# Performance work log

Hardware: AMD Instinct MI355X
Metric: run time of the kernel (lower is better)

## Reference

```python
import jax, jax.numpy as jnp
import numpy as np
from jax.ops import segment_sum, segment_max

N_NODES = 50000
N_GRAPHS = 64
EPS = 1e-16


def gat_layer(x, src, dst, W, a_src, a_dst, b, n_nodes):
    # PyG GATConv, heads=1: shared linear, additive attention, per-dst softmax
    h = x @ W                                  # [N, H]
    al_s = h @ a_src                           # [N]
    al_d = h @ a_dst                           # [N]
    e = jax.nn.leaky_relu(al_s[src] + al_d[dst], 0.2)   # [E]
    # numerically stable segment softmax over edges grouped by dst
    m = segment_max(e, dst, num_segments=n_nodes)
    m = jnp.where(jnp.isfinite(m), m, 0.0)
    ex = jnp.exp(e - m[dst])
    denom = segment_sum(ex, dst, num_segments=n_nodes)
    alpha = ex / (denom[dst] + EPS)            # [E]
    out = segment_sum(alpha[:, None] * h[src], dst, num_segments=n_nodes)
    return out + b


def setup_inputs() -> dict:
    key = jax.random.key(0)
    ks = jax.random.split(key, 16)
    H = 128
    x = jax.random.normal(ks[0], (N_NODES, 4), dtype=jnp.float32)
    edge_index = jax.random.randint(ks[1], (2, 800000), 0, N_NODES, dtype=jnp.int64)
    batch = jnp.sort(jax.random.randint(ks[2], (N_NODES,), 0, N_GRAPHS, dtype=jnp.int64))

    def glorot(k, shape):
        lim = np.sqrt(6.0 / (shape[0] + shape[-1]))
        return jax.random.uniform(k, shape, jnp.float32, -lim, lim)

    params = {
        'W1': glorot(ks[3], (4, H)), 'as1': glorot(ks[4], (H,)), 'ad1': glorot(ks[5], (H,)), 'b1': jnp.zeros((H,), jnp.float32),
        'W2': glorot(ks[6], (H, H)), 'as2': glorot(ks[7], (H,)), 'ad2': glorot(ks[8], (H,)), 'b2': jnp.zeros((H,), jnp.float32),
        'W3': glorot(ks[9], (H, H)), 'as3': glorot(ks[10], (H,)), 'ad3': glorot(ks[11], (H,)), 'b3': jnp.zeros((H,), jnp.float32),
        'Wlin': glorot(ks[12], (H, 2)), 'blin': jnp.zeros((2,), jnp.float32),
    }
    return {'x': x, 'edge_index': edge_index, 'batch': batch, **params}


def reference(x, edge_index, batch, W1, as1, ad1, b1, W2, as2, ad2, b2, W3, as3, ad3, b3, Wlin, blin):
    n = x.shape[0]
    # GATConv default add_self_loops=True
    loop = jnp.arange(n, dtype=edge_index.dtype)
    src = jnp.concatenate([edge_index[0], loop])
    dst = jnp.concatenate([edge_index[1], loop])

    h = jax.nn.relu(gat_layer(x, src, dst, W1, as1, ad1, b1, n))
    h = jax.nn.relu(gat_layer(h, src, dst, W2, as2, ad2, b2, n))
    h = gat_layer(h, src, dst, W3, as3, ad3, b3, n)

    # global_mean_pool
    sums = segment_sum(h, batch, num_segments=N_GRAPHS)          # [G, H]
    cnt = segment_sum(jnp.ones((n,), h.dtype), batch, num_segments=N_GRAPHS)
    pooled = sums / jnp.maximum(cnt, 1.0)[:, None]
    # dropout p=0.5 is identity in eval mode
    return pooled @ Wlin + blin                                   # [G, 2]
```

## Files before the change

### kernel.cpp

```cpp
#include <hip/hip_runtime.h>
#include <math.h>


#define BW 512
#define PART_CHUNK 4096

typedef __attribute__((ext_vector_type(8))) short short8v;
typedef __attribute__((ext_vector_type(4))) float f32x4;

__device__ __forceinline__ float bflo(unsigned u) { return __uint_as_float(u << 16); }
__device__ __forceinline__ float bfhi(unsigned u) { return __uint_as_float(u & 0xffff0000u); }
__device__ __forceinline__ unsigned pk2bf(float a, float b) {
  unsigned ua = __float_as_uint(a); ua += 0x7fffu + ((ua >> 16) & 1u);
  unsigned ub = __float_as_uint(b); ub += 0x7fffu + ((ub >> 16) & 1u);
  return (ua >> 16) | (ub & 0xffff0000u);
}

__global__ __launch_bounds__(256) void kb_hist(const int* __restrict__ ei,
                                               int* __restrict__ bcnt,
                                               int E, int ET, int NB) {
  __shared__ int h[128];
  int tid = threadIdx.x;
  if (tid < 128) h[tid] = 0;
  __syncthreads();
  int stride = gridDim.x * 256;
  for (int i = blockIdx.x * 256 + tid; i < ET; i += stride) {
    int dst = (i < E) ? ei[E + i] : (i - E);
    atomicAdd(&h[dst >> 9], 1);
  }
  __syncthreads();
  if (tid < NB && h[tid] > 0) atomicAdd(&bcnt[tid], h[tid]);
}

__global__ __launch_bounds__(128) void kb_scan(const int* __restrict__ bcnt,
                                               int* __restrict__ bbase,
                                               int* __restrict__ bcur,
                                               int* __restrict__ rowp,
                                               int N, int ET, int NB) {
  __shared__ int sm[128];
  int t = threadIdx.x;
  int v = (t < NB) ? bcnt[t] : 0;
  sm[t] = v;
  __syncthreads();
  for (int off = 1; off < 128; off <<= 1) {
    int u = (t >= off) ? sm[t - off] : 0;
    __syncthreads();
    sm[t] += u;
    __syncthreads();
  }
  int pre = sm[t] - v;
  if (t <= NB) bbase[t] = pre;
  if (t < NB) bcur[t] = pre;
  if (t == 0) rowp[N] = ET;
}

__global__ __launch_bounds__(256) void kb_part(const int* __restrict__ ei,
                                               int* __restrict__ bcur,
                                               int* __restrict__ bucketed,
                                               int E, int ET, int NB) {
  __shared__ int hist[128];
  __shared__ int runb[128];
  int tid = threadIdx.x;
  int base = blockIdx.x * PART_CHUNK;
  if (tid < 128) hist[tid] = 0;

  int sv[16], dv[16];
#pragma unroll
  for (int k = 0; k < 16; ++k) {
    int j = base + k * 256 + tid;
    int s = -1, d = 0;
    if (j < ET) {
      if (j < E) { s = ei[j]; d = ei[E + j]; }
      else       { s = j - E; d = j - E; }
    }
    sv[k] = s; dv[k] = d;
  }
  __syncthreads();
#pragma unroll
  for (int k = 0; k < 16; ++k)
    if (sv[k] >= 0) atomicAdd(&hist[dv[k] >> 9], 1);
  __syncthreads();
  if (tid < NB && hist[tid] > 0) runb[tid] = atomicAdd(&bcur[tid], hist[tid]);
  __syncthreads();
  if (tid < 128) hist[tid] = 0;
  __syncthreads();
#pragma unroll
  for (int k = 0; k < 16; ++k) {
    if (sv[k] >= 0) {
      int b = dv[k] >> 9;
      int off = atomicAdd(&hist[b], 1);
      bucketed[runb[b] + off] = (sv[k] << 9) | (dv[k] & (BW - 1));
    }
  }
}

__global__ __launch_bounds__(256) void kb_csr(const int* __restrict__ bucketed,
                                              const int* __restrict__ bbase,
                                              int* __restrict__ rowp,
                                              int* __restrict__ csr,
                                              int N) {
  __shared__ int h[512];
  __shared__ int sm[256];
  __shared__ int cur[512];
  int tid = threadIdx.x;
  int b = blockIdx.x;
  int cb = bbase[b], ce = bbase[b + 1];

  h[tid] = 0; h[tid + 256] = 0;
  __syncthreads();
  for (int j = cb + tid; j < ce; j += 256)
    atomicAdd(&h[bucketed[j] & (BW - 1)], 1);
  __syncthreads();
  int a0 = h[2 * tid], a1 = h[2 * tid + 1];
  int s = a0 + a1;
  sm[tid] = s;
  __syncthreads();
  for (int off = 1; off < 256; off <<= 1) {
    int u = (tid >= off) ? sm[tid - off] : 0;
    __syncthreads();
    sm[tid] += u;
    __syncthreads();
  }
  int pre = sm[tid] - s;
  cur[2 * tid] = pre;
  cur[2 * tid + 1] = pre + a0;
  __syncthreads();
  int node0 = b * BW;
  for (int local = tid; local < BW; local += 256) {
    int node = node0 + local;
    if (node < N) rowp[node] = cb + cur[local];
  }
  __syncthreads();
  for (int j = cb + tid; j < ce; j += 256) {
    int p = bucketed[j];
    int loc = p & (BW - 1);
    int pos = cb + atomicAdd(&cur[loc], 1);
    csr[pos] = (unsigned)p >> 9;
  }
}

__global__ __launch_bounds__(256) void k_prep(const float* __restrict__ W2,
                                              const float* __restrict__ W3,
                                              unsigned short* __restrict__ Wcm2,
                                              unsigned short* __restrict__ Wcm3) {
  int i = blockIdx.x * 256 + threadIdx.x;
  if (i < 16384) {
    int k = i >> 7, n = i & 127;
    unsigned u = __float_as_uint(W2[i]); u += 0x7fffu + ((u >> 16) & 1u);
    Wcm2[n * 128 + k] = (unsigned short)(u >> 16);
    unsigned v = __float_as_uint(W3[i]); v += 0x7fffu + ((v >> 16) & 1u);
    Wcm3[n * 128 + k] = (unsigned short)(v >> 16);
  }
}

__global__ __launch_bounds__(64) void k_al1(const float* __restrict__ W1,
                                            const float* __restrict__ as1,
                                            const float* __restrict__ ad1,
                                            float* __restrict__ wv) {
  int lane = threadIdx.x;
  float2 a = *(const float2*)(as1 + lane * 2);
  float2 d = *(const float2*)(ad1 + lane * 2);
  float ps[4], pd[4];
#pragma unroll
  for (int k = 0; k < 4; ++k) {
    float2 w = *(const float2*)(W1 + k * 128 + lane * 2);
    ps[k] = w.x * a.x + w.y * a.y;
    pd[k] = w.x * d.x + w.y * d.y;
  }
  for (int off = 32; off; off >>= 1) {
#pragma unroll
    for (int k = 0; k < 4; ++k) {
      ps[k] += __shfl_xor(ps[k], off);
      pd[k] += __shfl_xor(pd[k], off);
    }
  }
  if (lane == 0) {
#pragma unroll
    for (int k = 0; k < 4; ++k) { wv[k] = ps[k]; wv[4 + k] = pd[k]; }
  }
}

__global__ __launch_bounds__(256) void k_alnode(const float* __restrict__ X,
                                                const float* __restrict__ wv,
                                                float* __restrict__ al_s,
                                                float* __restrict__ al_d, int N) {
  int i = blockIdx.x * 256 + threadIdx.x;
  if (i >= N) return;
  float4 xv = *(const float4*)(X + i * 4);
  al_s[i] = xv.x * wv[0] + xv.y * wv[1] + xv.z * wv[2] + xv.w * wv[3];
  al_d[i] = xv.x * wv[4] + xv.y * wv[5] + xv.z * wv[6] + xv.w * wv[7];
}

__global__ __launch_bounds__(256) void k_aggx(const int* __restrict__ csr_src,
                                              const int* __restrict__ rowp,
                                              const float* __restrict__ al_s,
                                              const float* __restrict__ al_d,
                                              const float* __restrict__ X,
                                              float* __restrict__ exw,
                                              float* __restrict__ AX, int N) {
  int wid = threadIdx.x >> 6, lane = threadIdx.x & 63;
  int dst = blockIdx.x * 4 + wid;
  if (dst >= N) return;
  int beg = rowp[dst], end = rowp[dst + 1];
  int deg = end - beg;
  float ald = al_d[dst];
  float4 acc = {0.f, 0.f, 0.f, 0.f};

  if (deg <= 64) {
    int srcv = 0;
    float e = -INFINITY;
    if (lane < deg) {
      srcv = csr_src[beg + lane];
      e = al_s[srcv] + ald;
      e = (e > 0.f) ? e : 0.2f * e;
    }
    float m = e;
    for (int off = 32; off; off >>= 1) m = fmaxf(m, __shfl_xor(m, off));
    float av = (lane < deg) ? __expf(e - m) : 0.f;
    float den = av;
    for (int off = 32; off; off >>= 1) den += __shfl_xor(den, off);
    av *= 1.0f / (den + 1e-16f);
    float4 xv = {0.f, 0.f, 0.f, 0.f};
    if (lane < deg) xv = *(const float4*)(X + (size_t)srcv * 4);
    acc.x = av * xv.x; acc.y = av * xv.y; acc.z = av * xv.z; acc.w = av * xv.w;
  } else {
    float m = -INFINITY;
    for (int j = beg + lane; j < end; j += 64) {
      float e = al_s[csr_src[j]] + ald;
      e = (e > 0.f) ? e : 0.2f * e;
      exw[j] = e;
      m = fmaxf(m, e);
    }
    for (int off = 32; off; off >>= 1) m = fmaxf(m, __shfl_xor(m, off));
    float den = 0.f;
    for (int j = beg + lane; j < end; j += 64) {
      float ex = __expf(exw[j] - m);
      exw[j] = ex;
      den += ex;
    }
    for (int off = 32; off; off >>= 1) den += __shfl_xor(den, off);
    float inv = 1.0f / (den + 1e-16f);
    for (int j = beg + lane; j < end; j += 64) {
      int s = csr_src[j];
      float w = exw[j] * inv;
      float4 xv = *(const float4*)(X + (size_t)s * 4);
      acc.x += w * xv.x; acc.y += w * xv.y; acc.z += w * xv.z; acc.w += w * xv.w;
    }
  }
  for (int off = 32; off; off >>= 1) {
    acc.x += __shfl_xor(acc.x, off);
    acc.y += __shfl_xor(acc.y, off);
    acc.z += __shfl_xor(acc.z, off);
    acc.w += __shfl_xor(acc.w, off);
  }
  if (lane == 0) *(float4*)(AX + (size_t)dst * 4) = acc;
}

__global__ __launch_bounds__(256) void k_gemm4b(const float* __restrict__ AX,
                                                const float* __restrict__ W,
                                                const float* __restrict__ bias,
                                                unsigned* __restrict__ Ybf, int N) {
  int wid = threadIdx.x >> 6, lane = threadIdx.x & 63;
  int node = blockIdx.x * 4 + wid;
  if (node >= N) return;
  float4 xv = *(const float4*)(AX + (size_t)node * 4);
  int f = lane * 2;
  float2 w0 = *(const float2*)(W + f);
  float2 w1 = *(const float2*)(W + 128 + f);
  float2 w2 = *(const float2*)(W + 256 + f);
  float2 w3 = *(const float2*)(W + 384 + f);
  float2 bv = *(const float2*)(bias + f);
  float h0 = xv.x * w0.x + xv.y * w1.x + xv.z * w2.x + xv.w * w3.x + bv.x;
  float h1 = xv.x * w0.y + xv.y * w1.y + xv.z * w2.y + xv.w * w3.y + bv.y;
  h0 = fmaxf(h0, 0.f); h1 = fmaxf(h1, 0.f);
  Ybf[(size_t)node * 64 + lane] = pk2bf(h0, h1);
}

__global__ __launch_bounds__(256) void k_gemm128mfma(
    const unsigned short* __restrict__ Xbf,
    const unsigned short* __restrict__ Wcm,
    const float* __restrict__ asv, const float* __restrict__ adv,
    unsigned* __restrict__ Hbf,
    float* __restrict__ al_s, float* __restrict__ al_d, int N) {
  int wid = threadIdx.x >> 6, lane = threadIdx.x & 63;
  int c = lane & 15, g = lane >> 4;
  int row0 = blockIdx.x * 64 + wid * 16;
  int arow = row0 + c;
  int arowc = (arow < N) ? arow : (N - 1);

  short8v a[4];
#pragma unroll
  for (int kt = 0; kt < 4; ++kt)
    a[kt] = *(const short8v*)(Xbf + (size_t)arowc * 128 + kt * 32 + g * 8);

  f32x4 acc[8];
#pragma unroll
  for (int f = 0; f < 8; ++f) acc[f] = (f32x4){0.f, 0.f, 0.f, 0.f};

#pragma unroll
  for (int f = 0; f < 8; ++f) {
    const unsigned short* wb = Wcm + (size_t)(f * 16 + c) * 128 + g * 8;
#pragma unroll
    for (int kt = 0; kt < 4; ++kt) {
      short8v b = *(const short8v*)(wb + kt * 32);
      acc[f] = __builtin_amdgcn_mfma_f32_16x16x32_bf16(a[kt], b, acc[f], 0, 0, 0);
    }
  }

  float ps[4] = {0.f, 0.f, 0.f, 0.f}, pd[4] = {0.f, 0.f, 0.f, 0.f};
#pragma unroll
  for (int f = 0; f < 8; ++f) {
    float as_c = asv[f * 16 + c], ad_c = adv[f * 16 + c];
#pragma unroll
    for (int j = 0; j < 4; ++j) { ps[j] += acc[f][j] * as_c; pd[j] += acc[f][j] * ad_c; }
  }
#pragma unroll
  for (int j = 0; j < 4; ++j) {
    for (int off = 1; off < 16; off <<= 1) {
      ps[j] += __shfl_xor(ps[j], off);
      pd[j] += __shfl_xor(pd[j], off);
    }
  }
  if (c == 0) {
#pragma unroll
    for (int j = 0; j < 4; ++j) {
      int r = row0 + g * 4 + j;
      if (r < N) { al_s[r] = ps[j]; al_d[r] = pd[j]; }
    }
  }

#pragma unroll
  for (int f = 0; f < 8; ++f) {
#pragma unroll
    for (int j = 0; j < 4; ++j) {
      float partner = __shfl_xor(acc[f][j], 1);
      int r = row0 + g * 4 + j;
      if (((lane & 1) == 0) && r < N)
        Hbf[(size_t)r * 64 + f * 8 + (c >> 1)] = pk2bf(acc[f][j], partner);
    }
  }
}

__global__ __launch_bounds__(256) void k_agg(const int* __restrict__ csr_src,
                                             const int* __restrict__ rowp,
                                             const float* __restrict__ al_s,
                                             const float* __restrict__ al_d,
                                             const uint4* __restrict__ Hbf,
                                             const float* __restrict__ bias,
                                             float* __restrict__ exw,
                                             float* __restrict__ Yf32,
                                             uint4* __restrict__ Ybf,
                                             int N, int relu) {
  int wid = threadIdx.x >> 6, lane = threadIdx.x & 63;
  int dst = blockIdx.x * 4 + wid;
  if (dst >= N) return;
  int beg = rowp[dst], end = rowp[dst + 1];
  int deg = end - beg;
  float ald = al_d[dst];

  int q = lane >> 4;
  int l = lane & 15;
  float acc[8];
#pragma unroll
  for (int c = 0; c < 8; ++c) acc[c] = 0.f;

  if (deg <= 64) {
    int srcv = 0;
    float e = -INFINITY;
    if (lane < deg) {
      srcv = csr_src[beg + lane];
      e = al_s[srcv] + ald;
      e = (e > 0.f) ? e : 0.2f * e;
    }
    float m = e;
    for (int off = 32; off; off >>= 1) m = fmaxf(m, __shfl_xor(m, off));
    float av = (lane < deg) ? __expf(e - m) : 0.f;
    float den = av;
    for (int off = 32; off; off >>= 1) den += __shfl_xor(den, off);
    av *= 1.0f / (den + 1e-16f);

    int t = 0;
    for (; t + 16 <= deg; t += 16) {
      int s0 = __shfl(srcv, t + q);
      int s1 = __shfl(srcv, t + 4 + q);
      int s2 = __shfl(srcv, t + 8 + q);
      int s3 = __shfl(srcv, t + 12 + q);
      float w0 = __shfl(av, t + q);
      float w1 = __shfl(av, t + 4 + q);
      float w2 = __shfl(av, t + 8 + q);
      float w3 = __shfl(av, t + 12 + q);
      uint4 v0 = Hbf[(size_t)s0 * 16 + l];
      uint4 v1 = Hbf[(size_t)s1 * 16 + l];
      uint4 v2 = Hbf[(size_t)s2 * 16 + l];
      uint4 v3 = Hbf[(size_t)s3 * 16 + l];
      acc[0] += w0 * bflo(v0.x) + w1 * bflo(v1.x) + w2 * bflo(v2.x) + w3 * bflo(v3.x);
      acc[1] += w0 * bfhi(v0.x) + w1 * bfhi(v1.x) + w2 * bfhi(v2.x) + w3 * bfhi(v3.x);
      acc[2] += w0 * bflo(v0.y) + w1 * bflo(v1.y) + w2 * bflo(v2.y) + w3 * bflo(v3.y);
      acc[3] += w0 * bfhi(v0.y) + w1 * bfhi(v1.y) + w2 * bfhi(v2.y) + w3 * bfhi(v3.y);
      acc[4] += w0 * bflo(v0.z) + w1 * bflo(v1.z) + w2 * bflo(v2.z) + w3 * bflo(v3.z);
      acc[5] += w0 * bfhi(v0.z) + w1 * bfhi(v1.z) + w2 * bfhi(v2.z) + w3 * bfhi(v3.z);
      acc[6] += w0 * bflo(v0.w) + w1 * bflo(v1.w) + w2 * bflo(v2.w) + w3 * bflo(v3.w);
      acc[7] += w0 * bfhi(v0.w) + w1 * bfhi(v1.w) + w2 * bfhi(v2.w) + w3 * bfhi(v3.w);
    }
    if (t + 8 <= deg) {
      int sA = __shfl(srcv, t + q);
      int sB = __shfl(srcv, t + 4 + q);
      float wA = __shfl(av, t + q);
      float wB = __shfl(av, t + 4 + q);
      uint4 va = Hbf[(size_t)sA * 16 + l];
      uint4 vb = Hbf[(size_t)sB * 16 + l];
      acc[0] += wA * bflo(va.x) + wB * bflo(vb.x);
      acc[1] += wA * bfhi(va.x) + wB * bfhi(vb.x);
      acc[2] += wA * bflo(va.y) + wB * bflo(vb.y);
      acc[3] += wA * bfhi(va.y) + wB * bfhi(vb.y);
      acc[4] += wA * bflo(va.z) + wB * bflo(vb.z);
      acc[5] += wA * bfhi(va.z) + wB * bfhi(vb.z);
      acc[6] += wA * bflo(va.w) + wB * bflo(vb.w);
      acc[7] += wA * bfhi(va.w) + wB * bfhi(vb.w);
      t += 8;
    }
    if (t + 4 <= deg) {
      int sA = __shfl(srcv, t + q);
      float wA = __shfl(av, t + q);
      uint4 va = Hbf[(size_t)sA * 16 + l];
      acc[0] += wA * bflo(va.x); acc[1] += wA * bfhi(va.x);
      acc[2] += wA * bflo(va.y); acc[3] += wA * bfhi(va.y);
      acc[4] += wA * bflo(va.z); acc[5] += wA * bfhi(va.z);
      acc[6] += wA * bflo(va.w); acc[7] += wA * bfhi(va.w);
      t += 4;
    }
    {
      int sA = __shfl(srcv, t + q);
      float wA = __shfl(av, t + q);
      if (t + q < deg) {
        uint4 va = Hbf[(size_t)sA * 16 + l];
        acc[0] += wA * bflo(va.x); acc[1] += wA * bfhi(va.x);
        acc[2] += wA * bflo(va.y); acc[3] += wA * bfhi(va.y);
        acc[4] += wA * bflo(va.z); acc[5] += wA * bfhi(va.z);
        acc[6] += wA * bflo(va.w); acc[7] += wA * bfhi(va.w);
      }
    }
  } else {
    float m = -INFINITY;
    for (int j = beg + lane; j < end; j += 64) {
      float e = al_s[csr_src[j]] + ald;
      e = (e > 0.f) ? e : 0.2f * e;
      exw[j] = e;
      m = fmaxf(m, e);
    }
    for (int off = 32; off; off >>= 1) m = fmaxf(m, __shfl_xor(m, off));

    float den = 0.f;
    for (int j = beg + lane; j < end; j += 64) {
      float ex = __expf(exw[j] - m);
      exw[j] = ex;
      den += ex;
    }
    for (int off = 32; off; off >>= 1) den += __shfl_xor(den, off);
    float inv = 1.0f / (den + 1e-16f);

    for (int j = beg + q; j < end; j += 4) {
      int sA = csr_src[j];
      float wA = exw[j] * inv;
      uint4 va = Hbf[(size_t)sA * 16 + l];
      acc[0] += wA * bflo(va.x); acc[1] += wA * bfhi(va.x);
      acc[2] += wA * bflo(va.y); acc[3] += wA * bfhi(va.y);
      acc[4] += wA * bflo(va.z); acc[5] += wA * bfhi(va.z);
      acc[6] += wA * bflo(va.w); acc[7] += wA * bfhi(va.w);
    }
  }

#pragma unroll
  for (int c = 0; c < 8; ++c) {
    acc[c] += __shfl_xor(acc[c], 16);
    acc[c] += __shfl_xor(acc[c], 32);
  }
  if (q == 0) {
    float4 bv0 = *(const float4*)(bias + l * 8);
    float4 bv1 = *(const float4*)(bias + l * 8 + 4);
    float o0 = acc[0] + bv0.x, o1 = acc[1] + bv0.y, o2 = acc[2] + bv0.z, o3 = acc[3] + bv0.w;
    float o4 = acc[4] + bv1.x, o5 = acc[5] + bv1.y, o6 = acc[6] + bv1.z, o7 = acc[7] + bv1.w;
    if (relu) {
      o0 = fmaxf(o0, 0.f); o1 = fmaxf(o1, 0.f); o2 = fmaxf(o2, 0.f); o3 = fmaxf(o3, 0.f);
      o4 = fmaxf(o4, 0.f); o5 = fmaxf(o5, 0.f); o6 = fmaxf(o6, 0.f); o7 = fmaxf(o7, 0.f);
      uint4 pb;
      pb.x = pk2bf(o0, o1); pb.y = pk2bf(o2, o3);
      pb.z = pk2bf(o4, o5); pb.w = pk2bf(o6, o7);
      Ybf[(size_t)dst * 16 + l] = pb;
    } else {
      float4 w0 = make_float4(o0, o1, o2, o3);
      float4 w1 = make_float4(o4, o5, o6, o7);
      *(float4*)(Yf32 + (size_t)dst * 128 + l * 8) = w0;
      *(float4*)(Yf32 + (size_t)dst * 128 + l * 8 + 4) = w1;
    }
  }
}

__global__ __launch_bounds__(256) void k_pool(const float* __restrict__ Hh,
                                              const int* __restrict__ batch,
                                              float* __restrict__ gsum,
                                              float* __restrict__ gcnt,
                                              int N, int nwaves) {
  int gw = (blockIdx.x * 256 + threadIdx.x) >> 6;
  int lane = threadIdx.x & 63;
  int chunk = (N + nwaves - 1) / nwaves;
  int beg = gw * chunk;
  int end = beg + chunk; if (end > N) end = N;
  if (beg >= end) return;

  int curg = batch[beg];
  float2 acc = {0.f, 0.f};
  int cnt = 0;
  for (int n = beg; n < end; ++n) {
    int g = batch[n];
    if (g != curg) {
      atomicAdd(&gsum[curg * 128 + lane * 2], acc.x);
      atomicAdd(&gsum[curg * 128 + lane * 2 + 1], acc.y);
      if (lane == 0) atomicAdd(&gcnt[curg], (float)cnt);
      acc.x = 0.f; acc.y = 0.f; cnt = 0; curg = g;
    }
    float2 h = *(const float2*)(Hh + (size_t)n * 128 + lane * 2);
    acc.x += h.x; acc.y += h.y; ++cnt;
  }
  atomicAdd(&gsum[curg * 128 + lane * 2], acc.x);
  atomicAdd(&gsum[curg * 128 + lane * 2 + 1], acc.y);
  if (lane == 0) atomicAdd(&gcnt[curg], (float)cnt);
}

__global__ __launch_bounds__(128) void k_final(const float* __restrict__ gsum,
                                               const float* __restrict__ gcnt,
                                               const float* __restrict__ Wlin,
                                               const float* __restrict__ blin,
                                               float* __restrict__ out) {
  int t = threadIdx.x;
  int g = t >> 1, c = t & 1;
  float inv = 1.0f / fmaxf(gcnt[g], 1.0f);
  float acc = blin[c];
  for (int k = 0; k < 128; ++k) acc += gsum[g * 128 + k] * inv * Wlin[k * 2 + c];
  out[g * 2 + c] = acc;
}

extern "C" void kernel_launch(void* const* d_in, const int* in_sizes, int n_in,
                              void* d_out, int out_size, void* d_ws, size_t ws_size,
                              hipStream_t stream) {
  const float* x    = (const float*)d_in[0];
  const int*   ei   = (const int*)d_in[1];
  const int*   batch= (const int*)d_in[2];
  const float* W1   = (const float*)d_in[3];
  const float* as1  = (const float*)d_in[4];
  const float* ad1  = (const float*)d_in[5];
  const float* b1   = (const float*)d_in[6];
  const float* W2   = (const float*)d_in[7];
  const float* as2  = (const float*)d_in[8];
  const float* ad2  = (const float*)d_in[9];
  const float* b2   = (const float*)d_in[10];
  const float* W3   = (const float*)d_in[11];
  const float* as3  = (const float*)d_in[12];
  const float* ad3  = (const float*)d_in[13];
  const float* b3   = (const float*)d_in[14];
  const float* Wlin = (const float*)d_in[15];
  const float* blin = (const float*)d_in[16];

  int N = in_sizes[0] / 4;
  int E = in_sizes[1] / 2;
  int ET = E + N;
  int NB = (N + BW - 1) / BW;

  char* ws = (char*)d_ws;
  unsigned* bfA = (unsigned*)ws; ws += (size_t)N * 64 * 4;
  unsigned* bfB = (unsigned*)ws; ws += (size_t)N * 64 * 4;
  float* bufY = (float*)ws; ws += (size_t)N * 128 * 4;
  float* al_s = (float*)ws; ws += (size_t)N * 4;
  float* al_d = (float*)ws; ws += (size_t)N * 4;
  float* AX   = (float*)ws; ws += (size_t)N * 4 * 4;
  float* gsum = (float*)ws; ws += (size_t)64 * 128 * 4;
  float* gcnt = (float*)ws; ws += (size_t)64 * 4;
  float* wv   = (float*)ws; ws += (size_t)64 * 4;
  int* rowp   = (int*)ws;   ws += (size_t)(N + 1) * 4;
  int* csr    = (int*)ws;   ws += (size_t)ET * 4;
  float* exw  = (float*)ws; ws += (size_t)ET * 4;
  int* bucketed = (int*)ws; ws += (size_t)ET * 4;
  int* bcnt   = (int*)ws;   ws += (size_t)128 * 4;
  int* bbase  = (int*)ws;   ws += (size_t)132 * 4;
  int* bcur   = (int*)ws;   ws += (size_t)128 * 4;
  unsigned short* wcm2 = (unsigned short*)ws; ws += (size_t)128 * 128 * 2;
  unsigned short* wcm3 = (unsigned short*)ws; ws += (size_t)128 * 128 * 2;

  hipMemsetAsync(bcnt, 0, (size_t)128 * 4, stream);
  hipMemsetAsync(gsum, 0, (size_t)(64 * 128 + 64) * 4, stream);

  kb_hist<<<256, 256, 0, stream>>>(ei, bcnt, E, ET, NB);
  kb_scan<<<1, 128, 0, stream>>>(bcnt, bbase, bcur, rowp, N, ET, NB);
  kb_part<<<(ET + PART_CHUNK - 1) / PART_CHUNK, 256, 0, stream>>>(ei, bcur, bucketed, E, ET, NB);
  kb_csr <<<NB, 256, 0, stream>>>(bucketed, bbase, rowp, csr, N);
  k_prep <<<64, 256, 0, stream>>>(W2, W3, wcm2, wcm3);
  k_al1  <<<1, 64, 0, stream>>>(W1, as1, ad1, wv);

  int nb4 = (N + 3) / 4;
  int nb64 = (N + 63) / 64;
  k_alnode<<<(N + 255) / 256, 256, 0, stream>>>(x, wv, al_s, al_d, N);
  k_aggx  <<<nb4, 256, 0, stream>>>(csr, rowp, al_s, al_d, x, exw, AX, N);
  k_gemm4b<<<nb4, 256, 0, stream>>>(AX, W1, b1, bfB, N);
  k_gemm128mfma<<<nb64, 256, 0, stream>>>((const unsigned short*)bfB, wcm2, as2, ad2, bfA, al_s, al_d, N);
  k_agg        <<<nb4, 256, 0, stream>>>(csr, rowp, al_s, al_d, (const uint4*)bfA, b2, exw, bufY, (uint4*)bfB, N, 1);
  k_gemm128mfma<<<nb64, 256, 0, stream>>>((const unsigned short*)bfB, wcm3, as3, ad3, bfA, al_s, al_d, N);
  k_agg        <<<nb4, 256, 0, stream>>>(csr, rowp, al_s, al_d, (const uint4*)bfA, b3, exw, bufY, (uint4*)bfB, N, 0);

  k_pool <<<256, 256, 0, stream>>>(bufY, batch, gsum, gcnt, N, 1024);
  k_final<<<1, 128, 0, stream>>>(gsum, gcnt, Wlin, blin, (float*)d_out);
}
```

Before: 330.7 us.

## Fuse layer-1 gather with its linear, merge prep kernels, fuse pool and head

Folds the k_al1 wave into an extra block of k_prep and fuses layer-1 aggregation with the 4-to-128 linear, which removes the AX round trip and two launches. The final layer now writes bf16 instead of fp32, roughly halving that output's traffic. The atomic pool and final head kernels become one per-graph kernel that binary-searches the sorted batch array, so the memset and atomics go away. In exchange, pooling runs on bf16 activations at lower precision, and each graph is summed by a single block of 256 threads, which limits parallelism.

```diff
diff --git a/kernel.cpp b/kernel.cpp
--- a/kernel.cpp
+++ b/kernel.cpp
@@ -141,8 +141,37 @@
 
 __global__ __launch_bounds__(256) void k_prep(const float* __restrict__ W2,
                                               const float* __restrict__ W3,
+                                              const float* __restrict__ W1,
+                                              const float* __restrict__ as1,
+                                              const float* __restrict__ ad1,
                                               unsigned short* __restrict__ Wcm2,
-                                              unsigned short* __restrict__ Wcm3) {
+                                              unsigned short* __restrict__ Wcm3,
+                                              float* __restrict__ wv) {
+  if (blockIdx.x == 64) {
+    int lane = threadIdx.x;
+    if (lane >= 64) return;
+    float2 a = *(const float2*)(as1 + lane * 2);
+    float2 d = *(const float2*)(ad1 + lane * 2);
+    float ps[4], pd[4];
+#pragma unroll
+    for (int k = 0; k < 4; ++k) {
+      float2 w = *(const float2*)(W1 + k * 128 + lane * 2);
+      ps[k] = w.x * a.x + w.y * a.y;
+      pd[k] = w.x * d.x + w.y * d.y;
+    }
+    for (int off = 32; off; off >>= 1) {
+#pragma unroll
+      for (int k = 0; k < 4; ++k) {
+        ps[k] += __shfl_xor(ps[k], off);
+        pd[k] += __shfl_xor(pd[k], off);
+      }
+    }
+    if (lane == 0) {
+#pragma unroll
+      for (int k = 0; k < 4; ++k) { wv[k] = ps[k]; wv[4 + k] = pd[k]; }
+    }
+    return;
+  }
   int i = blockIdx.x * 256 + threadIdx.x;
   if (i < 16384) {
     int k = i >> 7, n = i & 127;
@@ -150,33 +179,6 @@
     Wcm2[n * 128 + k] = (unsigned short)(u >> 16);
     unsigned v = __float_as_uint(W3[i]); v += 0x7fffu + ((v >> 16) & 1u);
     Wcm3[n * 128 + k] = (unsigned short)(v >> 16);
-  }
-}
-
-__global__ __launch_bounds__(64) void k_al1(const float* __restrict__ W1,
-                                            const float* __restrict__ as1,
-                                            const float* __restrict__ ad1,
-                                            float* __restrict__ wv) {
-  int lane = threadIdx.x;
-  float2 a = *(const float2*)(as1 + lane * 2);
-  float2 d = *(const float2*)(ad1 + lane * 2);
-  float ps[4], pd[4];
-#pragma unroll
-  for (int k = 0; k < 4; ++k) {
-    float2 w = *(const float2*)(W1 + k * 128 + lane * 2);
-    ps[k] = w.x * a.x + w.y * a.y;
-    pd[k] = w.x * d.x + w.y * d.y;
-  }
-  for (int off = 32; off; off >>= 1) {
-#pragma unroll
-    for (int k = 0; k < 4; ++k) {
-      ps[k] += __shfl_xor(ps[k], off);
-      pd[k] += __shfl_xor(pd[k], off);
-    }
-  }
-  if (lane == 0) {
-#pragma unroll
-    for (int k = 0; k < 4; ++k) { wv[k] = ps[k]; wv[4 + k] = pd[k]; }
   }
 }
 
@@ -191,13 +193,15 @@
   al_d[i] = xv.x * wv[4] + xv.y * wv[5] + xv.z * wv[6] + xv.w * wv[7];
 }
 
-__global__ __launch_bounds__(256) void k_aggx(const int* __restrict__ csr_src,
-                                              const int* __restrict__ rowp,
-                                              const float* __restrict__ al_s,
-                                              const float* __restrict__ al_d,
-                                              const float* __restrict__ X,
-                                              float* __restrict__ exw,
-                                              float* __restrict__ AX, int N) {
+__global__ __launch_bounds__(256) void k_aggx1(const int* __restrict__ csr_src,
+                                               const int* __restrict__ rowp,
+                                               const float* __restrict__ al_s,
+                                               const float* __restrict__ al_d,
+                                               const float* __restrict__ X,
+                                               const float* __restrict__ W,
+                                               const float* __restrict__ bias,
+                                               float* __restrict__ exw,
+                                               unsigned* __restrict__ Ybf, int N) {
   int wid = threadIdx.x >> 6, lane = threadIdx.x & 63;
   int dst = blockIdx.x * 4 + wid;
   if (dst >= N) return;
@@ -253,27 +257,16 @@
     acc.z += __shfl_xor(acc.z, off);
     acc.w += __shfl_xor(acc.w, off);
   }
-  if (lane == 0) *(float4*)(AX + (size_t)dst * 4) = acc;
-}
-
-__global__ __launch_bounds__(256) void k_gemm4b(const float* __restrict__ AX,
-                                                const float* __restrict__ W,
-                                                const float* __restrict__ bias,
-                                                unsigned* __restrict__ Ybf, int N) {
-  int wid = threadIdx.x >> 6, lane = threadIdx.x & 63;
-  int node = blockIdx.x * 4 + wid;
-  if (node >= N) return;
-  float4 xv = *(const float4*)(AX + (size_t)node * 4);
   int f = lane * 2;
   float2 w0 = *(const float2*)(W + f);
   float2 w1 = *(const float2*)(W + 128 + f);
   float2 w2 = *(const float2*)(W + 256 + f);
   float2 w3 = *(const float2*)(W + 384 + f);
   float2 bv = *(const float2*)(bias + f);
-  float h0 = xv.x * w0.x + xv.y * w1.x + xv.z * w2.x + xv.w * w3.x + bv.x;
-  float h1 = xv.x * w0.y + xv.y * w1.y + xv.z * w2.y + xv.w * w3.y + bv.y;
+  float h0 = acc.x * w0.x + acc.y * w1.x + acc.z * w2.x + acc.w * w3.x + bv.x;
+  float h1 = acc.x * w0.y + acc.y * w1.y + acc.z * w2.y + acc.w * w3.y + bv.y;
   h0 = fmaxf(h0, 0.f); h1 = fmaxf(h1, 0.f);
-  Ybf[(size_t)node * 64 + lane] = pk2bf(h0, h1);
+  Ybf[(size_t)dst * 64 + lane] = pk2bf(h0, h1);
 }
 
 __global__ __launch_bounds__(256) void k_gemm128mfma(
@@ -348,7 +341,6 @@
                                              const uint4* __restrict__ Hbf,
                                              const float* __restrict__ bias,
                                              float* __restrict__ exw,
-                                             float* __restrict__ Yf32,
                                              uint4* __restrict__ Ybf,
                                              int N, int relu) {
   int wid = threadIdx.x >> 6, lane = threadIdx.x & 63;
@@ -483,61 +475,55 @@
     if (relu) {
       o0 = fmaxf(o0, 0.f); o1 = fmaxf(o1, 0.f); o2 = fmaxf(o2, 0.f); o3 = fmaxf(o3, 0.f);
       o4 = fmaxf(o4, 0.f); o5 = fmaxf(o5, 0.f); o6 = fmaxf(o6, 0.f); o7 = fmaxf(o7, 0.f);
-      uint4 pb;
-      pb.x = pk2bf(o0, o1); pb.y = pk2bf(o2, o3);
-      pb.z = pk2bf(o4, o5); pb.w = pk2bf(o6, o7);
-      Ybf[(size_t)dst * 16 + l] = pb;
-    } else {
-      float4 w0 = make_float4(o0, o1, o2, o3);
-      float4 w1 = make_float4(o4, o5, o6, o7);
-      *(float4*)(Yf32 + (size_t)dst * 128 + l * 8) = w0;
-      *(float4*)(Yf32 + (size_t)dst * 128 + l * 8 + 4) = w1;
-    }
-  }
-}
-
-__global__ __launch_bounds__(256) void k_pool(const float* __restrict__ Hh,
-                                              const int* __restrict__ batch,
-                                              float* __restrict__ gsum,
-                                              float* __restrict__ gcnt,
-                                              int N, int nwaves) {
-  int gw = (blockIdx.x * 256 + threadIdx.x) >> 6;
-  int lane = threadIdx.x & 63;
-  int chunk = (N + nwaves - 1) / nwaves;
-  int beg = gw * chunk;
-  int end = beg + chunk; if (end > N) end = N;
-  if (beg >= end) return;
-
-  int curg = batch[beg];
-  float2 acc = {0.f, 0.f};
-  int cnt = 0;
-  for (int n = beg; n < end; ++n) {
-    int g = batch[n];
-    if (g != curg) {
-      atomicAdd(&gsum[curg * 128 + lane * 2], acc.x);
-      atomicAdd(&gsum[curg * 128 + lane * 2 + 1], acc.y);
-      if (lane == 0) atomicAdd(&gcnt[curg], (float)cnt);
-      acc.x = 0.f; acc.y = 0.f; cnt = 0; curg = g;
-    }
-    float2 h = *(const float2*)(Hh + (size_t)n * 128 + lane * 2);
-    acc.x += h.x; acc.y += h.y; ++cnt;
-  }
-  atomicAdd(&gsum[curg * 128 + lane * 2], acc.x);
-  atomicAdd(&gsum[curg * 128 + lane * 2 + 1], acc.y);
-  if (lane == 0) atomicAdd(&gcnt[curg], (float)cnt);
-}
-
-__global__ __launch_bounds__(128) void k_final(const float* __restrict__ gsum,
-                                               const float* __restrict__ gcnt,
-                                               const float* __restrict__ Wlin,
-                                               const float* __restrict__ blin,
-                                               float* __restrict__ out) {
-  int t = threadIdx.x;
-  int g = t >> 1, c = t & 1;
-  float inv = 1.0f / fmaxf(gcnt[g], 1.0f);
-  float acc = blin[c];
-  for (int k = 0; k < 128; ++k) acc += gsum[g * 128 + k] * inv * Wlin[k * 2 + c];
-  out[g * 2 + c] = acc;
+    }
+    uint4 pb;
+    pb.x = pk2bf(o0, o1); pb.y = pk2bf(o2, o3);
+    pb.z = pk2bf(o4, o5); pb.w = pk2bf(o6, o7);
+    Ybf[(size_t)dst * 16 + l] = pb;
+  }
+}
+
+__global__ __launch_bounds__(256) void k_poolhead(const unsigned* __restrict__ Ybf,
+                                                  const int* __restrict__ batch,
+                                                  const float* __restrict__ Wlin,
+                                                  const float* __restrict__ blin,
+                                                  float* __restrict__ out, int N) {
+  __shared__ float gs[4][128];
+  __shared__ int bounds[2];
+  int tid = threadIdx.x, wid = tid >> 6, lane = tid & 63;
+  int g = blockIdx.x;
+  if (tid < 2) {
+    int target = g + tid;
+    int lo = 0, hi = N;
+    while (lo < hi) { int mid = (lo + hi) >> 1; if (batch[mid] < target) lo = mid + 1; else hi = mid; }
+    bounds[tid] = lo;
+  }
+  __syncthreads();
+  int beg = bounds[0], end = bounds[1];
+  float2 a = {0.f, 0.f};
+  for (int n = beg + wid; n < end; n += 4) {
+    unsigned u = Ybf[(size_t)n * 64 + lane];
+    a.x += bflo(u); a.y += bfhi(u);
+  }
+  gs[wid][lane * 2] = a.x;
+  gs[wid][lane * 2 + 1] = a.y;
+  __syncthreads();
+  if (wid == 0) {
+    int k0 = lane * 2, k1 = k0 + 1;
+    float inv = 1.0f / fmaxf((float)(end - beg), 1.0f);
+    float s0 = (gs[0][k0] + gs[1][k0] + gs[2][k0] + gs[3][k0]) * inv;
+    float s1 = (gs[0][k1] + gs[1][k1] + gs[2][k1] + gs[3][k1]) * inv;
+    float p0 = s0 * Wlin[k0 * 2] + s1 * Wlin[k1 * 2];
+    float p1 = s0 * Wlin[k0 * 2 + 1] + s1 * Wlin[k1 * 2 + 1];
+    for (int off = 32; off; off >>= 1) {
+      p0 += __shfl_xor(p0, off);
+      p1 += __shfl_xor(p1, off);
+    }
+    if (lane == 0) {
+      out[g * 2 + 0] = blin[0] + p0;
+      out[g * 2 + 1] = blin[1] + p1;
+    }
+  }
 }
 
 extern "C" void kernel_launch(void* const* d_in, const int* in_sizes, int n_in,
@@ -569,12 +555,8 @@
   char* ws = (char*)d_ws;
   unsigned* bfA = (unsigned*)ws; ws += (size_t)N * 64 * 4;
   unsigned* bfB = (unsigned*)ws; ws += (size_t)N * 64 * 4;
-  float* bufY = (float*)ws; ws += (size_t)N * 128 * 4;
   float* al_s = (float*)ws; ws += (size_t)N * 4;
   float* al_d = (float*)ws; ws += (size_t)N * 4;
-  float* AX   = (float*)ws; ws += (size_t)N * 4 * 4;
-  float* gsum = (float*)ws; ws += (size_t)64 * 128 * 4;
-  float* gcnt = (float*)ws; ws += (size_t)64 * 4;
   float* wv   = (float*)ws; ws += (size_t)64 * 4;
   int* rowp   = (int*)ws;   ws += (size_t)(N + 1) * 4;
   int* csr    = (int*)ws;   ws += (size_t)ET * 4;
@@ -587,25 +569,21 @@
   unsigned short* wcm3 = (unsigned short*)ws; ws += (size_t)128 * 128 * 2;
 
   hipMemsetAsync(bcnt, 0, (size_t)128 * 4, stream);
-  hipMemsetAsync(gsum, 0, (size_t)(64 * 128 + 64) * 4, stream);
 
   kb_hist<<<256, 256, 0, stream>>>(ei, bcnt, E, ET, NB);
   kb_scan<<<1, 128, 0, stream>>>(bcnt, bbase, bcur, rowp, N, ET, NB);
   kb_part<<<(ET + PART_CHUNK - 1) / PART_CHUNK, 256, 0, stream>>>(ei, bcur, bucketed, E, ET, NB);
   kb_csr <<<NB, 256, 0, stream>>>(bucketed, bbase, rowp, csr, N);
-  k_prep <<<64, 256, 0, stream>>>(W2, W3, wcm2, wcm3);
-  k_al1  <<<1, 64, 0, stream>>>(W1, as1, ad1, wv);
+  k_prep <<<65, 256, 0, stream>>>(W2, W3, W1, as1, ad1, wcm2, wcm3, wv);
 
   int nb4 = (N + 3) / 4;
   int nb64 = (N + 63) / 64;
   k_alnode<<<(N + 255) / 256, 256, 0, stream>>>(x, wv, al_s, al_d, N);
-  k_aggx  <<<nb4, 256, 0, stream>>>(csr, rowp, al_s, al_d, x, exw, AX, N);
-  k_gemm4b<<<nb4, 256, 0, stream>>>(AX, W1, b1, bfB, N);
+  k_aggx1 <<<nb4, 256, 0, stream>>>(csr, rowp, al_s, al_d, x, W1, b1, exw, bfB, N);
   k_gemm128mfma<<<nb64, 256, 0, stream>>>((const unsigned short*)bfB, wcm2, as2, ad2, bfA, al_s, al_d, N);
-  k_agg        <<<nb4, 256, 0, stream>>>(csr, rowp, al_s, al_d, (const uint4*)bfA, b2, exw, bufY, (uint4*)bfB, N, 1);
+  k_agg        <<<nb4, 256, 0, stream>>>(csr, rowp, al_s, al_d, (const uint4*)bfA, b2, exw, (uint4*)bfB, N, 1);
   k_gemm128mfma<<<nb64, 256, 0, stream>>>((const unsigned short*)bfB, wcm3, as3, ad3, bfA, al_s, al_d, N);
-  k_agg        <<<nb4, 256, 0, stream>>>(csr, rowp, al_s, al_d, (const uint4*)bfA, b3, exw, bufY, (uint4*)bfB, N, 0);
-
-  k_pool <<<256, 256, 0, stream>>>(bufY, batch, gsum, gcnt, N, 1024);
-  k_final<<<1, 128, 0, stream>>>(gsum, gcnt, Wlin, blin, (float*)d_out);
-}
+  k_agg        <<<nb4, 256, 0, stream>>>(csr, rowp, al_s, al_d, (const uint4*)bfA, b3, exw, (uint4*)bfB, N, 0);
+
+  k_poolhead<<<64, 256, 0, stream>>>(bfB, batch, Wlin, blin, (float*)d_out, N);
+}
```

Result: slower. 349.0 us (+5.5%).
